# Kernel tuning notes

Hardware: AMD Instinct MI355X
Metric: run time of the kernel (lower is better)

The kernel has to match this reference:

```python
import jax, jax.numpy as jnp
import numpy as np

N = 100_000      # nodes
E = 1_600_000    # directed edges
G = 512          # graphs in batch
IN, H, C = 26, 64, 2
EPS = 1e-5       # BatchNorm eps (torch default)


def setup_inputs() -> dict:
    key = jax.random.key(0)
    ks = jax.random.split(key, 12)
    s = 0.1
    return {
        "x": jax.random.normal(ks[0], (N, IN), jnp.float32),
        "edge_row": jax.random.randint(ks[1], (E,), 0, N, jnp.int32),
        "edge_col": jax.random.randint(ks[2], (E,), 0, N, jnp.int32),
        "batch": jnp.sort(jax.random.randint(ks[3], (N,), 0, G, jnp.int32)),
        "W0": jax.random.normal(ks[4], (IN, H), jnp.float32) * s,
        "b0": jnp.zeros((H,), jnp.float32),
        "W1": jax.random.normal(ks[5], (H, H), jnp.float32) * s,
        "b1": jnp.zeros((H,), jnp.float32),
        "W2": jax.random.normal(ks[6], (H, H), jnp.float32) * s,
        "b2": jnp.zeros((H,), jnp.float32),
        "bn_g": jnp.ones((3, H), jnp.float32),
        "bn_b": jnp.zeros((3, H), jnp.float32),
        "bn_m": jnp.zeros((3, H), jnp.float32),
        "bn_v": jnp.ones((3, H), jnp.float32),
        "Wc1": jax.random.normal(ks[7], (2 * H, H), jnp.float32) * s,
        "bc1": jnp.zeros((H,), jnp.float32),
        "Wc2": jax.random.normal(ks[8], (H, C), jnp.float32) * s,
        "bc2": jnp.zeros((C,), jnp.float32),
    }


def reference(x, edge_row, edge_col, batch, W0, b0, W1, b1, W2, b2,
              bn_g, bn_b, bn_m, bn_v, Wc1, bc1, Wc2, bc2):
    n = x.shape[0]
    # GCN normalization with self-loops (PyG gcn_norm)
    sl = jnp.arange(n, dtype=edge_row.dtype)
    row = jnp.concatenate([edge_row, sl])  # sources j
    col = jnp.concatenate([edge_col, sl])  # targets i
    deg = jax.ops.segment_sum(jnp.ones_like(row, jnp.float32), col, num_segments=n)
    dinv = jnp.where(deg > 0, jax.lax.rsqrt(deg), 0.0)
    norm = dinv[row] * dinv[col]  # [E+N]

    def conv(h, W, b):
        h = h @ W                                   # transform first (PyG)
        msg = h[row] * norm[:, None]                # gather + scale
        return jax.ops.segment_sum(msg, col, num_segments=n) + b  # scatter-add

    h = x
    for i, (W, b) in enumerate([(W0, b0), (W1, b1), (W2, b2)]):
        h = conv(h, W, b)
        # BatchNorm (eval: running stats) + ReLU; dropout off at inference
        h = (h - bn_m[i]) * jax.lax.rsqrt(bn_v[i] + EPS) * bn_g[i] + bn_b[i]
        h = jax.nn.relu(h)

    # global mean + max pool over batch vector
    cnt = jax.ops.segment_sum(jnp.ones((n, 1), h.dtype), batch, num_segments=G)
    mean = jax.ops.segment_sum(h, batch, num_segments=G) / jnp.maximum(cnt, 1.0)
    mx = jax.ops.segment_max(h, batch, num_segments=G)
    pooled = jnp.concatenate([mean, mx], axis=1)    # [G, 2H]

    hid = jax.nn.relu(pooled @ Wc1 + bc1)
    return hid @ Wc2 + bc2                          # [G, C]
```

## Files before the change

kernel.cpp:

```cpp
#include <hip/hip_runtime.h>

#define HDIM 64
#define EPSBN 1e-5f
#define MNODES 8
#define CAP 48
#define NB 256
#define BCAP 8192
#define EPB 2048
#define MAXW 400

typedef unsigned short u16;

__device__ __forceinline__ float bf2f(u16 b) {
    return __uint_as_float(((unsigned)b) << 16);
}
__device__ __forceinline__ u16 f2bf_rne(float f) {
    unsigned u = __float_as_uint(f);
    u += 0x7FFFu + ((u >> 16) & 1u);
    return (u16)(u >> 16);
}

__device__ __forceinline__ int bstart_of(int b, int N) {
    return (int)(((long long)b * N + NB - 1) / NB);
}

__global__ __launch_bounds__(256) void bucket_k(
    const int* __restrict__ row, const int* __restrict__ col,
    int* __restrict__ gcnt, int2* __restrict__ bstore, int E, int N,
    const int* __restrict__ batch, int* __restrict__ bounds, int G) {
    __shared__ int hist[NB];
    __shared__ int cur[NB];
    int tid = threadIdx.x;
    hist[tid] = 0;
    for (int i = blockIdx.x * 256 + tid; i < N; i += gridDim.x * 256) {
        int b = batch[i];
        int bp = (i == 0) ? -1 : batch[i - 1];
        for (int g = bp + 1; g <= b; g++) bounds[g] = i;
        if (i == N - 1) { for (int g = b + 1; g <= G; g++) bounds[g] = N; }
    }
    __syncthreads();
    int e0 = blockIdx.x * EPB;
    for (int u = 0; u < EPB / 256; u++) {
        int e = e0 + u * 256 + tid;
        if (e < E) {
            int c = __builtin_nontemporal_load(&col[e]);
            int b = (int)(((unsigned long long)c * NB) / (unsigned)N);
            atomicAdd(&hist[b], 1);
        }
    }
    __syncthreads();
    cur[tid] = atomicAdd(&gcnt[tid], hist[tid]);
    __syncthreads();
    for (int u = 0; u < EPB / 256; u++) {
        int e = e0 + u * 256 + tid;
        if (e < E) {
            int c = __builtin_nontemporal_load(&col[e]);
            int r = __builtin_nontemporal_load(&row[e]);
            int b = (int)(((unsigned long long)c * NB) / (unsigned)N);
            int slot = atomicAdd(&cur[b], 1);
            if (slot < BCAP) bstore[(size_t)b * BCAP + slot] = make_int2(r, c);
        }
    }
}

__global__ __launch_bounds__(256) void csrfill_k(
    const int* __restrict__ gcnt, const int2* __restrict__ bstore,
    int* __restrict__ cnt, int* __restrict__ esrcP,
    float* __restrict__ dinv, const float* __restrict__ x,
    u16* __restrict__ xp, int INR, int N) {
    __shared__ int lcnt[MAXW];
    int b = blockIdx.x, tid = threadIdx.x;
    int bs = bstart_of(b, N);
    int be = bstart_of(b + 1, N);
    int width = be - bs;
    for (int t = tid; t < width; t += 256) lcnt[t] = 0;
    __syncthreads();
    int M = min(gcnt[b], BCAP);
    const int2* bsp = bstore + (size_t)b * BCAP;
    for (int k = tid; k < M; k += 256) {
        int2 rc = bsp[k];
        int rank = atomicAdd(&lcnt[rc.y - bs], 1);
        if (rank < CAP) esrcP[rc.y * CAP + rank] = rc.x;
    }
    __syncthreads();
    for (int t = tid; t < width; t += 256) cnt[bs + t] = lcnt[t];
    for (int idx = tid; idx < width * 32; idx += 256) {
        int tl = idx >> 5, k = idx & 31;
        int i = bs + tl;
        float di = rsqrtf((float)min(lcnt[tl], CAP) + 1.0f);
        if (k == 0) dinv[i] = di;
        float xv = (k < INR) ? __builtin_nontemporal_load(&x[i * INR + k]) : 0.f;
        xp[i * 32 + k] = f2bf_rne(di * xv);
    }
}

template <int KIN, bool SCALEOUT>
__global__ __launch_bounds__(64) void conv_k(
    const u16* __restrict__ hb, const int* __restrict__ cnt,
    const int* __restrict__ esrcP, const float* __restrict__ dinv,
    const float* __restrict__ W, int KINR,
    const float* __restrict__ bias, const float* __restrict__ g,
    const float* __restrict__ bb, const float* __restrict__ m,
    const float* __restrict__ v, void* __restrict__ hout_, int n) {
    int lane = threadIdx.x;
    float wreg[KIN];
#pragma unroll
    for (int k = 0; k < KIN; k++) wreg[k] = (k < KINR) ? W[k * HDIM + lane] : 0.f;
    const float sc = g[lane] * rsqrtf(v[lane] + EPSBN);
    const float sh = (bias[lane] - m[lane]) * sc + bb[lane];

    __shared__ float agg4[4][KIN];

    const int feat = lane & (KIN - 1);
    auto ldh = [&](int node) -> float {
        return bf2f(hb[(size_t)node * KIN + feat]);
    };

    for (int grp = 0; grp < 2; grp++) {
        int ibase = blockIdx.x * MNODES + grp * 4;
        if (ibase >= n) break;
        float acc0 = 0.f, acc1 = 0.f, acc2 = 0.f, acc3 = 0.f;
        int e0 = 0, n0 = 0, e1 = 0, n1 = 0, e2 = 0, n2 = 0, e3 = 0, n3 = 0;
        {
            acc0 = ldh(ibase); e0 = ibase * CAP; n0 = e0 + min(cnt[ibase], CAP);
            if (ibase + 1 < n) { acc1 = ldh(ibase + 1); e1 = (ibase + 1) * CAP; n1 = e1 + min(cnt[ibase + 1], CAP); }
            if (ibase + 2 < n) { acc2 = ldh(ibase + 2); e2 = (ibase + 2) * CAP; n2 = e2 + min(cnt[ibase + 2], CAP); }
            if (ibase + 3 < n) { acc3 = ldh(ibase + 3); e3 = (ibase + 3) * CAP; n3 = e3 + min(cnt[ibase + 3], CAP); }
        }
        while (e0 + 2 <= n0 && e1 + 2 <= n1 && e2 + 2 <= n2 && e3 + 2 <= n3) {
            int s00 = esrcP[e0], s01 = esrcP[e0 + 1];
            int s10 = esrcP[e1], s11 = esrcP[e1 + 1];
            int s20 = esrcP[e2], s21 = esrcP[e2 + 1];
            int s30 = esrcP[e3], s31 = esrcP[e3 + 1];
            float h00 = ldh(s00), h01 = ldh(s01);
            float h10 = ldh(s10), h11 = ldh(s11);
            float h20 = ldh(s20), h21 = ldh(s21);
            float h30 = ldh(s30), h31 = ldh(s31);
            acc0 += h00 + h01;
            acc1 += h10 + h11;
            acc2 += h20 + h21;
            acc3 += h30 + h31;
            e0 += 2; e1 += 2; e2 += 2; e3 += 2;
        }
#define DRAIN(ek, nk, ak)                                                     \
        for (; ek + 4 <= nk; ek += 4) {                                       \
            int a = esrcP[ek], b = esrcP[ek + 1], c = esrcP[ek + 2], d = esrcP[ek + 3]; \
            float ha = ldh(a), hb2 = ldh(b), hc = ldh(c), hd = ldh(d);        \
            ak += (ha + hb2) + (hc + hd);                                     \
        }                                                                     \
        for (; ek < nk; ek++) ak += ldh(esrcP[ek]);
        DRAIN(e0, n0, acc0)
        DRAIN(e1, n1, acc1)
        DRAIN(e2, n2, acc2)
        DRAIN(e3, n3, acc3)
#undef DRAIN

        __syncthreads();
        if (lane < KIN) {
            agg4[0][lane] = acc0; agg4[1][lane] = acc1;
            agg4[2][lane] = acc2; agg4[3][lane] = acc3;
        }
        __syncthreads();
        for (int q = 0; q < 4; q++) {
            int i = ibase + q;
            if (i >= n) break;
            float di = dinv[i];
            float dot = 0.f;
            const float4* aggv = (const float4*)agg4[q];
#pragma unroll
            for (int k4 = 0; k4 < KIN / 4; k4++) {
                float4 a = aggv[k4];
                dot = fmaf(a.x, wreg[4 * k4 + 0], dot);
                dot = fmaf(a.y, wreg[4 * k4 + 1], dot);
                dot = fmaf(a.z, wreg[4 * k4 + 2], dot);
                dot = fmaf(a.w, wreg[4 * k4 + 3], dot);
            }
            float y = fmaxf(fmaf(dot * di, sc, sh), 0.f);
            if (SCALEOUT) ((u16*)hout_)[(size_t)i * HDIM + lane] = f2bf_rne(di * y);
            else          ((float*)hout_)[(size_t)i * HDIM + lane] = y;
        }
    }
}

__global__ __launch_bounds__(256) void pool_mlp_k(
    const float* __restrict__ h, const int* __restrict__ bounds,
    const float* __restrict__ Wc1, const float* __restrict__ bc1,
    const float* __restrict__ Wc2, const float* __restrict__ bc2,
    float* __restrict__ out, int n) {
    int gidx = blockIdx.x;
    int tid = threadIdx.x;
    int lane = tid & 63;
    int wv = tid >> 6;

    int start = bounds[gidx], end = bounds[gidx + 1];

    float sum = 0.f, mx = 0.f;
    for (int i = start + wv; i < end; i += 4) {
        float val = h[(size_t)i * HDIM + lane];
        sum += val;
        mx = fmaxf(mx, val);
    }
    __shared__ float ssum[4 * HDIM];
    __shared__ float smax[4 * HDIM];
    __shared__ float pooled[2 * HDIM];
    ssum[wv * HDIM + lane] = sum;
    smax[wv * HDIM + lane] = mx;
    __syncthreads();
    if (wv == 0) {
        float sv = ssum[lane] + ssum[64 + lane] + ssum[128 + lane] + ssum[192 + lane];
        float mm = fmaxf(fmaxf(smax[lane], smax[64 + lane]),
                         fmaxf(smax[128 + lane], smax[192 + lane]));
        int cntg = end - start;
        pooled[lane] = sv / fmaxf((float)cntg, 1.f);
        pooled[HDIM + lane] = mm;
    }
    __syncthreads();
    if (wv == 0) {
        float a = bc1[lane];
#pragma unroll
        for (int k = 0; k < 2 * HDIM; k++) a = fmaf(pooled[k], Wc1[k * HDIM + lane], a);
        a = fmaxf(a, 0.f);
#pragma unroll
        for (int c = 0; c < 2; c++) {
            float vv = a * Wc2[lane * 2 + c];
            for (int off = 32; off; off >>= 1) vv += __shfl_down(vv, off);
            if (lane == 0) out[gidx * 2 + c] = vv + bc2[c];
        }
    }
}

extern "C" void kernel_launch(void* const* d_in, const int* in_sizes, int n_in,
                              void* d_out, int out_size, void* d_ws, size_t ws_size,
                              hipStream_t stream) {
    const float* x    = (const float*)d_in[0];
    const int*   erow = (const int*)d_in[1];
    const int*   ecol = (const int*)d_in[2];
    const int*   batch= (const int*)d_in[3];
    const float* W0   = (const float*)d_in[4];
    const float* b0   = (const float*)d_in[5];
    const float* W1   = (const float*)d_in[6];
    const float* b1   = (const float*)d_in[7];
    const float* W2   = (const float*)d_in[8];
    const float* b2   = (const float*)d_in[9];
    const float* bn_g = (const float*)d_in[10];
    const float* bn_b = (const float*)d_in[11];
    const float* bn_m = (const float*)d_in[12];
    const float* bn_v = (const float*)d_in[13];
    const float* Wc1  = (const float*)d_in[14];
    const float* bc1  = (const float*)d_in[15];
    const float* Wc2  = (const float*)d_in[16];
    const float* bc2  = (const float*)d_in[17];
    float* out = (float*)d_out;

    const int N = in_sizes[3];
    const int E = in_sizes[1];
    const int G = out_size / 2;
    const int INR = in_sizes[0] / N;

    char* ws = (char*)d_ws;
    size_t off = 0;
    auto alloc = [&](size_t bytes) -> void* {
        void* p = ws + off;
        off += (bytes + 255) & ~(size_t)255;
        return p;
    };
    int*   gcnt   = (int*)alloc(NB * 4);
    int*   cnt    = (int*)alloc((size_t)N * 4);
    float* dinv   = (float*)alloc((size_t)N * 4);
    int*   bounds = (int*)alloc((size_t)(512 + 1) * 4);
    int2*  bstore = (int2*)alloc((size_t)NB * BCAP * 8);
    int*   esrcP  = (int*)alloc((size_t)N * CAP * 4);
    void*  bufA   = alloc((size_t)N * HDIM * 4);
    void*  bufB   = alloc((size_t)N * HDIM * 4);
    (void)ws_size;

    hipMemsetAsync(gcnt, 0, NB * 4, stream);
    int nbk = (E + EPB - 1) / EPB;
    bucket_k<<<nbk, 256, 0, stream>>>(erow, ecol, gcnt, bstore, E, N, batch, bounds, G);
    csrfill_k<<<NB, 256, 0, stream>>>(gcnt, bstore, cnt, esrcP, dinv, x, (u16*)bufB, INR, N);

    int cgrid = (N + MNODES - 1) / MNODES;
    conv_k<32, true><<<cgrid, 64, 0, stream>>>((const u16*)bufB, cnt, esrcP, dinv, W0, INR, b0,
        bn_g + 0, bn_b + 0, bn_m + 0, bn_v + 0, bufA, N);
    conv_k<64, true><<<cgrid, 64, 0, stream>>>((const u16*)bufA, cnt, esrcP, dinv, W1, 64, b1,
        bn_g + 64, bn_b + 64, bn_m + 64, bn_v + 64, bufB, N);
    conv_k<64, false><<<cgrid, 64, 0, stream>>>((const u16*)bufB, cnt, esrcP, dinv, W2, 64, b2,
        bn_g + 128, bn_b + 128, bn_m + 128, bn_v + 128, bufA, N);

    pool_mlp_k<<<G, 256, 0, stream>>>((const float*)bufA, bounds, Wc1, bc1, Wc2, bc2, out, N);
}
```

Measured before the change: 423.9 us.

## Replace padded per-node edge slots with compact CSR via block prefix scans

The fixed-capacity padded adjacency (CAP slots per node) becomes a compact CSR. Offsets are computed with a global scan over bucket counts and a local scan over per-node counts inside csrfill_k. Edges are then written in a second pass into a dense array sized E, and the conv kernels read offsets instead of i*CAP. The aim is to shrink the adjacency footprint and improve locality of edge index reads in the gather loops, at the cost of an extra pass over the bucket store and several block-wide scans with many barriers.

```diff
diff --git a/kernel.cpp b/kernel.cpp
--- a/kernel.cpp
+++ b/kernel.cpp
@@ -65,25 +65,53 @@
 
 __global__ __launch_bounds__(256) void csrfill_k(
     const int* __restrict__ gcnt, const int2* __restrict__ bstore,
-    int* __restrict__ cnt, int* __restrict__ esrcP,
+    int* __restrict__ offs, int* __restrict__ cnt, int* __restrict__ esrc,
     float* __restrict__ dinv, const float* __restrict__ x,
     u16* __restrict__ xp, int INR, int N) {
     __shared__ int lcnt[MAXW];
+    __shared__ int lrk[MAXW];
+    __shared__ int pref[MAXW];
+    __shared__ int sc[256];
     int b = blockIdx.x, tid = threadIdx.x;
     int bs = bstart_of(b, N);
     int be = bstart_of(b + 1, N);
     int width = be - bs;
-    for (int t = tid; t < width; t += 256) lcnt[t] = 0;
+
+    int gv = min(gcnt[tid], BCAP);
+    sc[tid] = gv;
+    __syncthreads();
+    for (int o = 1; o < 256; o <<= 1) {
+        int t2 = (tid >= o) ? sc[tid - o] : 0;
+        __syncthreads();
+        sc[tid] += t2;
+        __syncthreads();
+    }
+    int base = (b == 0) ? 0 : sc[b - 1];
+
+    for (int t = tid; t < width; t += 256) { lcnt[t] = 0; lrk[t] = 0; }
     __syncthreads();
     int M = min(gcnt[b], BCAP);
     const int2* bsp = bstore + (size_t)b * BCAP;
-    for (int k = tid; k < M; k += 256) {
-        int2 rc = bsp[k];
-        int rank = atomicAdd(&lcnt[rc.y - bs], 1);
-        if (rank < CAP) esrcP[rc.y * CAP + rank] = rc.x;
-    }
-    __syncthreads();
-    for (int t = tid; t < width; t += 256) cnt[bs + t] = lcnt[t];
+    for (int k = tid; k < M; k += 256) atomicAdd(&lcnt[bsp[k].y - bs], 1);
+    __syncthreads();
+    int c0 = (2 * tid     < width) ? min(lcnt[2 * tid],     CAP) : 0;
+    int c1 = (2 * tid + 1 < width) ? min(lcnt[2 * tid + 1], CAP) : 0;
+    sc[tid] = c0 + c1;
+    __syncthreads();
+    for (int o = 1; o < 256; o <<= 1) {
+        int t2 = (tid >= o) ? sc[tid - o] : 0;
+        __syncthreads();
+        sc[tid] += t2;
+        __syncthreads();
+    }
+    int pairExcl = sc[tid] - (c0 + c1);
+    if (2 * tid     < width) pref[2 * tid]     = pairExcl;
+    if (2 * tid + 1 < width) pref[2 * tid + 1] = pairExcl + c0;
+    __syncthreads();
+    for (int t = tid; t < width; t += 256) {
+        offs[bs + t] = base + pref[t];
+        cnt[bs + t] = min(lcnt[t], CAP);
+    }
     for (int idx = tid; idx < width * 32; idx += 256) {
         int tl = idx >> 5, k = idx & 31;
         int i = bs + tl;
@@ -92,12 +120,19 @@
         float xv = (k < INR) ? __builtin_nontemporal_load(&x[i * INR + k]) : 0.f;
         xp[i * 32 + k] = f2bf_rne(di * xv);
     }
+    for (int k = tid; k < M; k += 256) {
+        int2 rc = bsp[k];
+        int l = rc.y - bs;
+        int rank = atomicAdd(&lrk[l], 1);
+        if (rank < CAP) esrc[base + pref[l] + rank] = rc.x;
+    }
 }
 
 template <int KIN, bool SCALEOUT>
 __global__ __launch_bounds__(64) void conv_k(
-    const u16* __restrict__ hb, const int* __restrict__ cnt,
-    const int* __restrict__ esrcP, const float* __restrict__ dinv,
+    const u16* __restrict__ hb, const int* __restrict__ offs,
+    const int* __restrict__ cnt, const int* __restrict__ esrc,
+    const float* __restrict__ dinv,
     const float* __restrict__ W, int KINR,
     const float* __restrict__ bias, const float* __restrict__ g,
     const float* __restrict__ bb, const float* __restrict__ m,
@@ -122,16 +157,16 @@
         float acc0 = 0.f, acc1 = 0.f, acc2 = 0.f, acc3 = 0.f;
         int e0 = 0, n0 = 0, e1 = 0, n1 = 0, e2 = 0, n2 = 0, e3 = 0, n3 = 0;
         {
-            acc0 = ldh(ibase); e0 = ibase * CAP; n0 = e0 + min(cnt[ibase], CAP);
-            if (ibase + 1 < n) { acc1 = ldh(ibase + 1); e1 = (ibase + 1) * CAP; n1 = e1 + min(cnt[ibase + 1], CAP); }
-            if (ibase + 2 < n) { acc2 = ldh(ibase + 2); e2 = (ibase + 2) * CAP; n2 = e2 + min(cnt[ibase + 2], CAP); }
-            if (ibase + 3 < n) { acc3 = ldh(ibase + 3); e3 = (ibase + 3) * CAP; n3 = e3 + min(cnt[ibase + 3], CAP); }
+            acc0 = ldh(ibase); e0 = offs[ibase]; n0 = e0 + cnt[ibase];
+            if (ibase + 1 < n) { acc1 = ldh(ibase + 1); e1 = offs[ibase + 1]; n1 = e1 + cnt[ibase + 1]; }
+            if (ibase + 2 < n) { acc2 = ldh(ibase + 2); e2 = offs[ibase + 2]; n2 = e2 + cnt[ibase + 2]; }
+            if (ibase + 3 < n) { acc3 = ldh(ibase + 3); e3 = offs[ibase + 3]; n3 = e3 + cnt[ibase + 3]; }
         }
         while (e0 + 2 <= n0 && e1 + 2 <= n1 && e2 + 2 <= n2 && e3 + 2 <= n3) {
-            int s00 = esrcP[e0], s01 = esrcP[e0 + 1];
-            int s10 = esrcP[e1], s11 = esrcP[e1 + 1];
-            int s20 = esrcP[e2], s21 = esrcP[e2 + 1];
-            int s30 = esrcP[e3], s31 = esrcP[e3 + 1];
+            int s00 = esrc[e0], s01 = esrc[e0 + 1];
+            int s10 = esrc[e1], s11 = esrc[e1 + 1];
+            int s20 = esrc[e2], s21 = esrc[e2 + 1];
+            int s30 = esrc[e3], s31 = esrc[e3 + 1];
             float h00 = ldh(s00), h01 = ldh(s01);
             float h10 = ldh(s10), h11 = ldh(s11);
             float h20 = ldh(s20), h21 = ldh(s21);
@@ -144,11 +179,11 @@
         }
 #define DRAIN(ek, nk, ak)                                                     \
         for (; ek + 4 <= nk; ek += 4) {                                       \
-            int a = esrcP[ek], b = esrcP[ek + 1], c = esrcP[ek + 2], d = esrcP[ek + 3]; \
+            int a = esrc[ek], b = esrc[ek + 1], c = esrc[ek + 2], d = esrc[ek + 3]; \
             float ha = ldh(a), hb2 = ldh(b), hc = ldh(c), hd = ldh(d);        \
             ak += (ha + hb2) + (hc + hd);                                     \
         }                                                                     \
-        for (; ek < nk; ek++) ak += ldh(esrcP[ek]);
+        for (; ek < nk; ek++) ak += ldh(esrc[ek]);
         DRAIN(e0, n0, acc0)
         DRAIN(e1, n1, acc1)
         DRAIN(e2, n2, acc2)
@@ -265,11 +300,12 @@
         return p;
     };
     int*   gcnt   = (int*)alloc(NB * 4);
+    int*   offs   = (int*)alloc((size_t)N * 4);
     int*   cnt    = (int*)alloc((size_t)N * 4);
     float* dinv   = (float*)alloc((size_t)N * 4);
     int*   bounds = (int*)alloc((size_t)(512 + 1) * 4);
     int2*  bstore = (int2*)alloc((size_t)NB * BCAP * 8);
-    int*   esrcP  = (int*)alloc((size_t)N * CAP * 4);
+    int*   esrc   = (int*)alloc((size_t)E * 4 + 256);
     void*  bufA   = alloc((size_t)N * HDIM * 4);
     void*  bufB   = alloc((size_t)N * HDIM * 4);
     (void)ws_size;
@@ -277,14 +313,14 @@
     hipMemsetAsync(gcnt, 0, NB * 4, stream);
     int nbk = (E + EPB - 1) / EPB;
     bucket_k<<<nbk, 256, 0, stream>>>(erow, ecol, gcnt, bstore, E, N, batch, bounds, G);
-    csrfill_k<<<NB, 256, 0, stream>>>(gcnt, bstore, cnt, esrcP, dinv, x, (u16*)bufB, INR, N);
+    csrfill_k<<<NB, 256, 0, stream>>>(gcnt, bstore, offs, cnt, esrc, dinv, x, (u16*)bufB, INR, N);
 
     int cgrid = (N + MNODES - 1) / MNODES;
-    conv_k<32, true><<<cgrid, 64, 0, stream>>>((const u16*)bufB, cnt, esrcP, dinv, W0, INR, b0,
+    conv_k<32, true><<<cgrid, 64, 0, stream>>>((const u16*)bufB, offs, cnt, esrc, dinv, W0, INR, b0,
         bn_g + 0, bn_b + 0, bn_m + 0, bn_v + 0, bufA, N);
-    conv_k<64, true><<<cgrid, 64, 0, stream>>>((const u16*)bufA, cnt, esrcP, dinv, W1, 64, b1,
+    conv_k<64, true><<<cgrid, 64, 0, stream>>>((const u16*)bufA, offs, cnt, esrc, dinv, W1, 64, b1,
         bn_g + 64, bn_b + 64, bn_m + 64, bn_v + 64, bufB, N);
-    conv_k<64, false><<<cgrid, 64, 0, stream>>>((const u16*)bufB, cnt, esrcP, dinv, W2, 64, b2,
+    conv_k<64, false><<<cgrid, 64, 0, stream>>>((const u16*)bufB, offs, cnt, esrc, dinv, W2, 64, b2,
         bn_g + 128, bn_b + 128, bn_m + 128, bn_v + 128, bufA, N);
 
     pool_mlp_k<<<G, 256, 0, stream>>>((const float*)bufA, bounds, Wc1, bc1, Wc2, bc2, out, N);
```

New measurement: 386.5 us. 8.8% less time.
